# Performance work log

Measured on AMD Instinct MI355X. Metric: run time of the kernel, lower is better.

Reference implementation:

```python
import jax, jax.numpy as jnp
import numpy as np
import math

NLAT, NLON, LMAX, MMAX = 128, 256, 50, 50
K = 3  # three_nn

# ---- precompute: Clenshaw-Curtis quadrature (torch_harmonics 'equiangular') ----
def _cc_nodes_weights(n):
    Nn = n - 1
    theta = np.pi * np.arange(n) / Nn
    v = np.zeros(n)
    for k in range(1, Nn // 2 + 1):
        b = 1.0 if 2 * k == Nn else 2.0
        v += b * np.cos(2 * k * theta) / (4 * k * k - 1)
    w = (2.0 / Nn) * (1.0 - v)
    w[0] *= 0.5
    w[-1] *= 0.5
    return np.cos(theta), w

# ---- precompute: orthonormal associated Legendre P_l^m(cos theta), csphase ----
def _legpoly(lmax, mmax, cost):
    sint = np.sqrt(np.clip(1.0 - cost ** 2, 0.0, None))
    p = np.zeros((mmax, lmax, cost.shape[0]))
    pmm = np.full(cost.shape[0], np.sqrt(1.0 / (4.0 * np.pi)))
    for m in range(mmax):
        if m > 0:
            pmm = -pmm * np.sqrt((2.0 * m + 1.0) / (2.0 * m)) * sint
        p[m, m] = pmm
        if m + 1 < lmax:
            p[m, m + 1] = np.sqrt(2.0 * m + 3.0) * cost * pmm
        for l in range(m + 2, lmax):
            a = np.sqrt((4.0 * l * l - 1.0) / (l * l - m * m))
            b = np.sqrt(((2.0 * l + 1.0) * (l - 1 + m) * (l - 1 - m)) / ((2.0 * l - 3.0) * (l * l - m * m)))
            p[m, l] = a * cost * p[m, l - 1] - b * p[m, l - 2]
    return p

_cost, _w = _cc_nodes_weights(NLAT)
_PCTW = jnp.asarray((_legpoly(LMAX, MMAX, _cost) * _w[None, None, :]).astype(np.float32))  # (mmax,lmax,nlat)

_gx, _gy = np.meshgrid(np.arange(NLAT), np.arange(-NLAT, NLAT), indexing='ij')
_GRID = jnp.asarray((np.stack([_gx.ravel(), _gy.ravel()], -1) / NLAT * np.pi).astype(np.float32))  # (M,2)

_RECTW = jnp.asarray(np.exp(-(LMAX - np.arange(1, LMAX + 1)) ** 2 / (2.0 * LMAX ** 2)).astype(np.float32))  # (lmax,)


def to_spherical(coords):
    # coords: (B,N,3) -> r:(B,N), sph:(B,N,2) = [arccos(x/r), azimuth in [0,2pi)]
    sq = coords ** 2
    pn = jnp.sqrt(jnp.flip(jnp.cumsum(jnp.flip(sq, -1), -1), -1))  # pn[...,i] = ||coords[...,i:]||
    r = pn[..., 0]
    phi = jnp.arccos(coords[..., :-2] / pn[..., :-2])
    a = jnp.arccos(coords[..., -2] / pn[..., -2])
    phi_final = a + (2.0 * math.pi - 2.0 * a) * (coords[..., -1] < 0)
    return r, jnp.concatenate([phi, phi_final[..., None]], axis=-1)


def interp_to_grid(coords):
    # spherical transform + 3-NN (squared dists) + distance-weighted interpolation onto the lat/lon grid
    r, sph = to_spherical(coords)
    sph = sph.at[..., 1].add(-math.pi)
    # brute-force pairwise squared distances grid(M,2) vs sph(B,N,2): (B,M,N)
    d2 = (jnp.sum(_GRID ** 2, -1)[None, :, None] + jnp.sum(sph ** 2, -1)[:, None, :]
          - 2.0 * jnp.einsum('md,bnd->bmn', _GRID, sph))
    _, idx = jax.lax.top_k(-jax.lax.stop_gradient(d2), K)  # (B,M,K), ascending distance
    sel = jax.vmap(lambda s, i: s[i])(sph, idx)            # (B,M,K,2)
    fsel = jax.vmap(lambda f, i: f[i])(r, idx)             # (B,M,K)
    dk = jnp.sum((_GRID[None, :, None, :] - sel) ** 2, -1)  # recompute selected sq-dists (differentiable)
    w = dk / jnp.sum(dk, -1, keepdims=True)                # weights = dist / sum(dist), as in source
    return jnp.sum(fsel * w, -1).reshape(-1, NLAT, NLON)


def sht_real(x):
    # RealSHT (equiangular, ortho): rfft(norm='forward')*2pi, then Legendre*quadrature einsum; real part only
    xf = jnp.fft.rfft(x, axis=-1)[..., :MMAX] * (2.0 * math.pi / NLON)
    return jnp.einsum('bkm,mlk->blm', jnp.real(xf).astype(jnp.float32), _PCTW)  # (B,lmax,mmax)


def setup_inputs() -> dict:
    key = jax.random.key(0)
    k1, k2 = jax.random.split(key)
    pred = jax.random.normal(k1, (2, 2048, 3), dtype=jnp.float32)
    target = jax.random.normal(k2, (2, 2048, 3), dtype=jnp.float32)
    return {"pred": pred, "target": target}


def reference(pred, target):
    pc = sht_real(interp_to_grid(pred))
    tc = sht_real(interp_to_grid(target))
    return jnp.mean(jnp.sum((pc - tc) ** 2 * _RECTW[None, :, None], axis=(1, 2)))
```

## Files before the change

### kernel.cpp

```cpp
#include <hip/hip_runtime.h>
#include <math.h>

#define PI_D 3.14159265358979323846
#define PIF  3.14159265358979323846f
#define NLAT 128
#define NLON 256
#define LMAX 50
#define MMAX 50
#define NPTS 2048
#define NBT 16
#define NBA 32
#define NBIN (NBT * NBA)
#define WBIN 0.19634954084936207f
#define INVW 5.092958178940651f
#define BIG 1e30f
#define KMASK 0xFFFFF800u

__device__ float g_pctwT[(size_t)LMAX * NLAT * MMAX];
__device__ float g_fre[(size_t)4 * NLAT * MMAX];

__device__ __forceinline__ void insert3(float kf, float& k0, float& k1, float& k2) {
    float n1 = __builtin_amdgcn_fmed3f(kf, k0, k1);
    float n2 = __builtin_amdgcn_fmed3f(kf, k1, k2);
    k0 = fminf(kf, k0);
    k1 = n1;
    k2 = n2;
}

__device__ __forceinline__ float mkkey(float gt, float gl, float2 tl, int idx) {
    float dt = gt - tl.x, dl = gl - tl.y;
    float d = fmaf(dt, dt, dl * dl);
    return __uint_as_float((__float_as_uint(d) & KMASK) | (unsigned)idx);
}

__global__ __launch_bounds__(1024) void fused_main(
    const float* __restrict__ pred, const float* __restrict__ tgt,
    float* __restrict__ out) {

    __shared__ float2 s_btl[NPTS];
    __shared__ float  s_br[NPTS];
    __shared__ int    s_cnt[NBIN];
    __shared__ int    s_off[NBIN + 1];
    __shared__ float  s_row[4][NLON];
    __shared__ float  s_part[4][256];

    int bid = blockIdx.x;
    int t = threadIdx.x;

    if (bid >= 128) {
        int k = bid - 128;
        int m = t;
        if (k == 0 && m == 0) out[0] = 0.0f;
        if (m >= MMAX) return;

        double thd = PI_D * (double)k / 127.0;
        float cost = (float)cos(thd);
        float sint = (float)sin(thd);

        float c2 = (float)cos(2.0 * thd);
        float two_c2 = 2.0f * c2;
        float cp = 1.0f, cc = c2, v = 0.0f;
        for (int tt = 1; tt <= 63; ++tt) {
            v += 2.0f * cc / (float)(4 * tt * tt - 1);
            float cn = two_c2 * cc - cp;
            cp = cc;
            cc = cn;
        }
        float w = (2.0f / 127.0f) * (1.0f - v);
        if (k == 0 || k == 127) w *= 0.5f;

        float pmm = sqrtf(1.0f / (4.0f * PIF));
        for (int i = 1; i <= m; ++i)
            pmm = -pmm * sqrtf((2.0f * (float)i + 1.0f) / (2.0f * (float)i)) * sint;

        float* o = g_pctwT + (size_t)k * MMAX + m;
        for (int l = 0; l < m; ++l) o[(size_t)l * NLAT * MMAX] = 0.0f;
        o[(size_t)m * NLAT * MMAX] = pmm * w;
        float plm2 = pmm, plm1 = 0.0f;
        if (m + 1 < LMAX) {
            plm1 = sqrtf(2.0f * (float)m + 3.0f) * cost * pmm;
            o[(size_t)(m + 1) * NLAT * MMAX] = plm1 * w;
        }
        for (int l = m + 2; l < LMAX; ++l) {
            float fl = (float)l;
            float denom = fl * fl - (float)(m * m);
            float a = sqrtf((4.0f * fl * fl - 1.0f) / denom);
            float b = sqrtf(((2.0f * fl + 1.0f) * (float)(l - 1 + m) * (float)(l - 1 - m)) /
                            ((2.0f * fl - 3.0f) * denom));
            float p = a * cost * plm1 - b * plm2;
            o[(size_t)l * NLAT * MMAX] = p * w;
            plm2 = plm1;
            plm1 = p;
        }
        return;
    }

    int f = bid >> 5;
    int latb = bid & 31;
    const float* src = ((f < 2) ? pred : tgt) + (size_t)(f & 1) * NPTS * 3;

    if (t < NBIN) s_cnt[t] = 0;
    __syncthreads();

    float pth[2], paz[2], pr[2];
    int pbin[2];
#pragma unroll
    for (int i = 0; i < 2; ++i) {
        int n = t + 1024 * i;
        float x = src[3 * n], y = src[3 * n + 1], z = src[3 * n + 2];
        float s1 = z * z;
        float s2 = s1 + y * y;
        float s3 = s2 + x * x;
        float r = sqrtf(s3);
        float rho = sqrtf(s2);
        float th = acosf(x / r);
        float a = acosf(y / rho);
        float az = (z < 0.0f) ? (a + (2.0f * PIF - 2.0f * a)) : a;
        az -= PIF;
        int bt = min(max((int)(th * INVW), 0), NBT - 1);
        int ba = min(max((int)((az + PIF) * INVW), 0), NBA - 1);
        int b = bt * NBA + ba;
        pth[i] = th; paz[i] = az; pr[i] = r; pbin[i] = b;
        atomicAdd(&s_cnt[b], 1);
    }
    __syncthreads();

    if (t == 0) s_off[NBIN] = NPTS;
    if (t < 64) {
        int base = t * 8;
        int loc[8];
        int run = 0;
#pragma unroll
        for (int i = 0; i < 8; ++i) { loc[i] = run; run += s_cnt[base + i]; }
        int x = run;
#pragma unroll
        for (int d = 1; d < 64; d <<= 1) {
            int y = __shfl_up(x, d);
            if (t >= d) x += y;
        }
        int ex = x - run;
#pragma unroll
        for (int i = 0; i < 8; ++i) s_off[base + i] = ex + loc[i];
    }
    __syncthreads();
    if (t < NBIN) s_cnt[t] = s_off[t];
    __syncthreads();
#pragma unroll
    for (int i = 0; i < 2; ++i) {
        int pos = atomicAdd(&s_cnt[pbin[i]], 1);
        s_btl[pos] = make_float2(pth[i], paz[i]);
        s_br[pos] = pr[i];
    }
    __syncthreads();

    int rl = t >> 8;
    int j = t & 255;
    int lat = latb + 32 * rl;
    float gt = (float)((double)lat * PI_D / 128.0);
    float gl = (float)(((double)j - 128.0) * PI_D / 128.0);
    float glp = gl + PIF;
    int bt0 = lat >> 3;
    int ba0 = j >> 3;

    auto scan_seg = [&](int i, int i1, float& q0, float& q1, float& q2) {
        for (; i + 4 <= i1; i += 4) {
            float2 a0 = s_btl[i];
            float2 a1 = s_btl[i + 1];
            float2 a2 = s_btl[i + 2];
            float2 a3 = s_btl[i + 3];
            insert3(mkkey(gt, gl, a0, i), q0, q1, q2);
            insert3(mkkey(gt, gl, a1, i + 1), q0, q1, q2);
            insert3(mkkey(gt, gl, a2, i + 2), q0, q1, q2);
            insert3(mkkey(gt, gl, a3, i + 3), q0, q1, q2);
        }
        for (; i < i1; ++i)
            insert3(mkkey(gt, gl, s_btl[i], i), q0, q1, q2);
    };

    float k0 = BIG, k1 = BIG, k2 = BIG;
    {
        int rtl = max(bt0 - 1, 0), rth = min(bt0 + 1, NBT - 1);
        int bal = max(ba0 - 1, 0), bah = min(ba0 + 1, NBA - 1);
        for (int bt = rtl; bt <= rth; ++bt)
            scan_seg(s_off[bt * NBA + bal], s_off[bt * NBA + bah + 1], k0, k1, k2);
    }

    bool done;
    {
        float safe = BIG;
        if (bt0 - 1 > 0)       safe = fminf(safe, gt - (float)(bt0 - 1) * WBIN);
        if (bt0 + 1 < NBT - 1) safe = fminf(safe, (float)(bt0 + 2) * WBIN - gt);
        if (ba0 - 1 > 0)       safe = fminf(safe, glp - (float)(ba0 - 1) * WBIN);
        if (ba0 + 1 < NBA - 1) safe = fminf(safe, (float)(ba0 + 2) * WBIN - glp);
        done = (k2 <= safe * safe);
    }

    for (int R = 2; R <= 31; ++R) {
        if (__all(done)) break;
        if (!done) {
            int btl = bt0 - R, bth = bt0 + R;
            int lo = max(btl, 0), hi = min(bth, NBT - 1);
            int bal = max(ba0 - R, 0), bah = min(ba0 + R, NBA - 1);
            for (int bt = lo; bt <= hi; ++bt) {
                if (bt == btl || bt == bth) {
                    scan_seg(s_off[bt * NBA + bal], s_off[bt * NBA + bah + 1], k0, k1, k2);
                } else {
                    if (ba0 - R >= 0) {
                        int b = bt * NBA + ba0 - R;
                        scan_seg(s_off[b], s_off[b + 1], k0, k1, k2);
                    }
                    if (ba0 + R <= NBA - 1) {
                        int b = bt * NBA + ba0 + R;
                        scan_seg(s_off[b], s_off[b + 1], k0, k1, k2);
                    }
                }
            }
            float safe = BIG;
            if (bt0 - R > 0)       safe = fminf(safe, gt - (float)(bt0 - R) * WBIN);
            if (bt0 + R < NBT - 1) safe = fminf(safe, (float)(bt0 + R + 1) * WBIN - gt);
            if (ba0 - R > 0)       safe = fminf(safe, glp - (float)(ba0 - R) * WBIN);
            if (ba0 + R < NBA - 1) safe = fminf(safe, (float)(ba0 + R + 1) * WBIN - glp);
            if (k2 <= safe * safe) done = true;
        }
    }

    {
        int i0 = __float_as_uint(k0) & 0x7FF;
        int i1 = __float_as_uint(k1) & 0x7FF;
        int i2 = __float_as_uint(k2) & 0x7FF;
        float2 p0 = s_btl[i0];
        float2 p1 = s_btl[i1];
        float2 p2 = s_btl[i2];
        float dt0 = gt - p0.x, dl0 = gl - p0.y;
        float dt1 = gt - p1.x, dl1 = gl - p1.y;
        float dt2 = gt - p2.x, dl2 = gl - p2.y;
        float d0 = fmaf(dt0, dt0, dl0 * dl0);
        float d1 = fmaf(dt1, dt1, dl1 * dl1);
        float d2 = fmaf(dt2, dt2, dl2 * dl2);
        float s = d0 + d1 + d2;
        s_row[rl][j] = (d0 * s_br[i0] + d1 * s_br[i1] + d2 * s_br[i2]) / s;
    }
    __syncthreads();

    {
        int q = (t >> 6) & 3;
        int mm = t & 63;
        if (mm < MMAX) {
            int bs = q * 64;
            const float W0 = 2.0f * PIF / 256.0f;
            float cphi2 = 2.0f * __cosf(W0 * (float)mm);
            float acc = 0.0f;
#pragma unroll
            for (int seg = 0; seg < 4; ++seg) {
                int i0 = bs + seg * 16;
                float c0 = __cosf(W0 * (float)((i0 * mm) & 255));
                float c1 = __cosf(W0 * (float)(((i0 + 1) * mm) & 255));
                acc = fmaf(s_row[rl][i0], c0, acc);
                acc = fmaf(s_row[rl][i0 + 1], c1, acc);
#pragma unroll
                for (int i = 2; i < 16; ++i) {
                    float cn = fmaf(cphi2, c1, -c0);
                    acc = fmaf(s_row[rl][i0 + i], cn, acc);
                    c0 = c1;
                    c1 = cn;
                }
            }
            s_part[rl][q * 64 + mm] = acc;
        }
    }
    __syncthreads();
    {
        int mm = t & 255;
        if (mm < MMAX) {
            const float* pp = s_part[rl];
            float v = ((pp[mm] + pp[64 + mm]) + (pp[128 + mm] + pp[192 + mm])) *
                      (float)(2.0 * PI_D / (double)NLON);
            g_fre[(f * NLAT + lat) * MMAX + mm] = v;
        }
    }
}

__global__ __launch_bounds__(256) void contract_loss(float* __restrict__ out) {
    int b = blockIdx.x / LMAX;
    int l = blockIdx.x % LMAX;
    int mm = threadIdx.x & 63;
    int kq = threadIdx.x >> 6;
    __shared__ float sp[4][64], st_[4][64];
    float pc = 0.0f, tc = 0.0f;
    if (mm < MMAX) {
        const float* pw = g_pctwT + ((size_t)l * NLAT + kq * 32) * MMAX + mm;
        const float* fp = g_fre + ((size_t)b * NLAT + kq * 32) * MMAX + mm;
        const float* ft = g_fre + ((size_t)(2 + b) * NLAT + kq * 32) * MMAX + mm;
#pragma unroll 8
        for (int k = 0; k < 32; ++k) {
            float w = pw[k * MMAX];
            pc += fp[k * MMAX] * w;
            tc += ft[k * MMAX] * w;
        }
    }
    sp[kq][mm] = pc;
    st_[kq][mm] = tc;
    __syncthreads();
    if (threadIdx.x < 64) {
        int m2 = threadIdx.x;
        float pcs = (sp[0][m2] + sp[1][m2]) + (sp[2][m2] + sp[3][m2]);
        float tcs = (st_[0][m2] + st_[1][m2]) + (st_[2][m2] + st_[3][m2]);
        float diff = pcs - tcs;
        double dl_ = (double)(49 - l);
        float rw = (float)exp(-(dl_ * dl_) / 5000.0);
        float contrib = (m2 < MMAX) ? diff * diff * rw * 0.5f : 0.0f;
        for (int off = 32; off > 0; off >>= 1) contrib += __shfl_down(contrib, off);
        if (m2 == 0) atomicAdd(out, contrib);
    }
}

extern "C" void kernel_launch(void* const* d_in, const int* in_sizes, int n_in,
                              void* d_out, int out_size, void* d_ws, size_t ws_size,
                              hipStream_t stream) {
    const float* pred = (const float*)d_in[0];
    const float* tgt = (const float*)d_in[1];
    float* out = (float*)d_out;
    (void)d_ws; (void)ws_size;

    fused_main<<<256, 1024, 0, stream>>>(pred, tgt, out);
    contract_loss<<<2 * LMAX, 256, 0, stream>>>(out);
}
```

Baseline: 79.17 us.

## Merge contraction into main kernel using a software grid barrier

Folds the contract_loss kernel into the main kernel. All 256 blocks meet at a global atomic arrive/spin barrier, after which the first 100 blocks do the Legendre contraction and loss reduction. The departure counter resets the barrier for the next call. This removes the second kernel launch and its launch gap. In exchange it depends on all 256 blocks of 1024 threads being co-resident, which should hold on MI355X's 256 CUs but is not guaranteed, and it adds spin-wait and fence costs.

```diff
diff --git a/kernel.cpp b/kernel.cpp
--- a/kernel.cpp
+++ b/kernel.cpp
@@ -19,6 +19,9 @@
 __device__ float g_pctwT[(size_t)LMAX * NLAT * MMAX];
 __device__ float g_fre[(size_t)4 * NLAT * MMAX];
 
+__device__ int g_arrive = 0;
+__device__ int g_depart = 0;
+
 __device__ __forceinline__ void insert3(float kf, float& k0, float& k1, float& k2) {
     float n1 = __builtin_amdgcn_fmed3f(kf, k0, k1);
     float n2 = __builtin_amdgcn_fmed3f(kf, k1, k2);
@@ -33,7 +36,7 @@
     return __uint_as_float((__float_as_uint(d) & KMASK) | (unsigned)idx);
 }
 
-__global__ __launch_bounds__(1024) void fused_main(
+__global__ __launch_bounds__(1024) void fused_all(
     const float* __restrict__ pred, const float* __restrict__ tgt,
     float* __restrict__ out) {
 
@@ -43,6 +46,7 @@
     __shared__ int    s_off[NBIN + 1];
     __shared__ float  s_row[4][NLON];
     __shared__ float  s_part[4][256];
+    __shared__ float  sp[4][64], st2[4][64];
 
     int bid = blockIdx.x;
     int t = threadIdx.x;
@@ -51,266 +55,286 @@
         int k = bid - 128;
         int m = t;
         if (k == 0 && m == 0) out[0] = 0.0f;
-        if (m >= MMAX) return;
-
-        double thd = PI_D * (double)k / 127.0;
-        float cost = (float)cos(thd);
-        float sint = (float)sin(thd);
-
-        float c2 = (float)cos(2.0 * thd);
-        float two_c2 = 2.0f * c2;
-        float cp = 1.0f, cc = c2, v = 0.0f;
-        for (int tt = 1; tt <= 63; ++tt) {
-            v += 2.0f * cc / (float)(4 * tt * tt - 1);
-            float cn = two_c2 * cc - cp;
-            cp = cc;
-            cc = cn;
-        }
-        float w = (2.0f / 127.0f) * (1.0f - v);
-        if (k == 0 || k == 127) w *= 0.5f;
-
-        float pmm = sqrtf(1.0f / (4.0f * PIF));
-        for (int i = 1; i <= m; ++i)
-            pmm = -pmm * sqrtf((2.0f * (float)i + 1.0f) / (2.0f * (float)i)) * sint;
-
-        float* o = g_pctwT + (size_t)k * MMAX + m;
-        for (int l = 0; l < m; ++l) o[(size_t)l * NLAT * MMAX] = 0.0f;
-        o[(size_t)m * NLAT * MMAX] = pmm * w;
-        float plm2 = pmm, plm1 = 0.0f;
-        if (m + 1 < LMAX) {
-            plm1 = sqrtf(2.0f * (float)m + 3.0f) * cost * pmm;
-            o[(size_t)(m + 1) * NLAT * MMAX] = plm1 * w;
-        }
-        for (int l = m + 2; l < LMAX; ++l) {
-            float fl = (float)l;
-            float denom = fl * fl - (float)(m * m);
-            float a = sqrtf((4.0f * fl * fl - 1.0f) / denom);
-            float b = sqrtf(((2.0f * fl + 1.0f) * (float)(l - 1 + m) * (float)(l - 1 - m)) /
-                            ((2.0f * fl - 3.0f) * denom));
-            float p = a * cost * plm1 - b * plm2;
-            o[(size_t)l * NLAT * MMAX] = p * w;
-            plm2 = plm1;
-            plm1 = p;
-        }
-        return;
+        if (m < MMAX) {
+            double thd = PI_D * (double)k / 127.0;
+            float cost = (float)cos(thd);
+            float sint = (float)sin(thd);
+
+            float c2 = (float)cos(2.0 * thd);
+            float two_c2 = 2.0f * c2;
+            float cp = 1.0f, cc = c2, v = 0.0f;
+            for (int tt = 1; tt <= 63; ++tt) {
+                v += 2.0f * cc / (float)(4 * tt * tt - 1);
+                float cn = two_c2 * cc - cp;
+                cp = cc;
+                cc = cn;
+            }
+            float w = (2.0f / 127.0f) * (1.0f - v);
+            if (k == 0 || k == 127) w *= 0.5f;
+
+            float pmm = sqrtf(1.0f / (4.0f * PIF));
+            for (int i = 1; i <= m; ++i)
+                pmm = -pmm * sqrtf((2.0f * (float)i + 1.0f) / (2.0f * (float)i)) * sint;
+
+            float* o = g_pctwT + (size_t)k * MMAX + m;
+            for (int l = 0; l < m; ++l) o[(size_t)l * NLAT * MMAX] = 0.0f;
+            o[(size_t)m * NLAT * MMAX] = pmm * w;
+            float plm2 = pmm, plm1 = 0.0f;
+            if (m + 1 < LMAX) {
+                plm1 = sqrtf(2.0f * (float)m + 3.0f) * cost * pmm;
+                o[(size_t)(m + 1) * NLAT * MMAX] = plm1 * w;
+            }
+            for (int l = m + 2; l < LMAX; ++l) {
+                float fl = (float)l;
+                float denom = fl * fl - (float)(m * m);
+                float a = sqrtf((4.0f * fl * fl - 1.0f) / denom);
+                float b = sqrtf(((2.0f * fl + 1.0f) * (float)(l - 1 + m) * (float)(l - 1 - m)) /
+                                ((2.0f * fl - 3.0f) * denom));
+                float p = a * cost * plm1 - b * plm2;
+                o[(size_t)l * NLAT * MMAX] = p * w;
+                plm2 = plm1;
+                plm1 = p;
+            }
+        }
+    } else {
+        int f = bid >> 5;
+        int latb = bid & 31;
+        const float* src = ((f < 2) ? pred : tgt) + (size_t)(f & 1) * NPTS * 3;
+
+        if (t < NBIN) s_cnt[t] = 0;
+        __syncthreads();
+
+        float pth[2], paz[2], pr[2];
+        int pbin[2];
+#pragma unroll
+        for (int i = 0; i < 2; ++i) {
+            int n = t + 1024 * i;
+            float x = src[3 * n], y = src[3 * n + 1], z = src[3 * n + 2];
+            float s1 = z * z;
+            float s2 = s1 + y * y;
+            float s3 = s2 + x * x;
+            float r = sqrtf(s3);
+            float rho = sqrtf(s2);
+            float th = acosf(x / r);
+            float a = acosf(y / rho);
+            float az = (z < 0.0f) ? (a + (2.0f * PIF - 2.0f * a)) : a;
+            az -= PIF;
+            int bt = min(max((int)(th * INVW), 0), NBT - 1);
+            int ba = min(max((int)((az + PIF) * INVW), 0), NBA - 1);
+            int b = bt * NBA + ba;
+            pth[i] = th; paz[i] = az; pr[i] = r; pbin[i] = b;
+            atomicAdd(&s_cnt[b], 1);
+        }
+        __syncthreads();
+
+        if (t == 0) s_off[NBIN] = NPTS;
+        if (t < 64) {
+            int base = t * 8;
+            int loc[8];
+            int run = 0;
+#pragma unroll
+            for (int i = 0; i < 8; ++i) { loc[i] = run; run += s_cnt[base + i]; }
+            int x = run;
+#pragma unroll
+            for (int d = 1; d < 64; d <<= 1) {
+                int y = __shfl_up(x, d);
+                if (t >= d) x += y;
+            }
+            int ex = x - run;
+#pragma unroll
+            for (int i = 0; i < 8; ++i) s_off[base + i] = ex + loc[i];
+        }
+        __syncthreads();
+        if (t < NBIN) s_cnt[t] = s_off[t];
+        __syncthreads();
+#pragma unroll
+        for (int i = 0; i < 2; ++i) {
+            int pos = atomicAdd(&s_cnt[pbin[i]], 1);
+            s_btl[pos] = make_float2(pth[i], paz[i]);
+            s_br[pos] = pr[i];
+        }
+        __syncthreads();
+
+        int rl = t >> 8;
+        int j = t & 255;
+        int lat = latb + 32 * rl;
+        float gt = (float)((double)lat * PI_D / 128.0);
+        float gl = (float)(((double)j - 128.0) * PI_D / 128.0);
+        float glp = gl + PIF;
+        int bt0 = lat >> 3;
+        int ba0 = j >> 3;
+
+        auto scan_seg = [&](int i, int i1, float& q0, float& q1, float& q2) {
+            for (; i + 4 <= i1; i += 4) {
+                float2 a0 = s_btl[i];
+                float2 a1 = s_btl[i + 1];
+                float2 a2 = s_btl[i + 2];
+                float2 a3 = s_btl[i + 3];
+                insert3(mkkey(gt, gl, a0, i), q0, q1, q2);
+                insert3(mkkey(gt, gl, a1, i + 1), q0, q1, q2);
+                insert3(mkkey(gt, gl, a2, i + 2), q0, q1, q2);
+                insert3(mkkey(gt, gl, a3, i + 3), q0, q1, q2);
+            }
+            for (; i < i1; ++i)
+                insert3(mkkey(gt, gl, s_btl[i], i), q0, q1, q2);
+        };
+
+        float k0 = BIG, k1 = BIG, k2 = BIG;
+        {
+            int rtl = max(bt0 - 1, 0), rth = min(bt0 + 1, NBT - 1);
+            int bal = max(ba0 - 1, 0), bah = min(ba0 + 1, NBA - 1);
+            for (int bt = rtl; bt <= rth; ++bt)
+                scan_seg(s_off[bt * NBA + bal], s_off[bt * NBA + bah + 1], k0, k1, k2);
+        }
+
+        bool done;
+        {
+            float safe = BIG;
+            if (bt0 - 1 > 0)       safe = fminf(safe, gt - (float)(bt0 - 1) * WBIN);
+            if (bt0 + 1 < NBT - 1) safe = fminf(safe, (float)(bt0 + 2) * WBIN - gt);
+            if (ba0 - 1 > 0)       safe = fminf(safe, glp - (float)(ba0 - 1) * WBIN);
+            if (ba0 + 1 < NBA - 1) safe = fminf(safe, (float)(ba0 + 2) * WBIN - glp);
+            done = (k2 <= safe * safe);
+        }
+
+        for (int R = 2; R <= 31; ++R) {
+            if (__all(done)) break;
+            if (!done) {
+                int btl = bt0 - R, bth = bt0 + R;
+                int lo = max(btl, 0), hi = min(bth, NBT - 1);
+                int bal = max(ba0 - R, 0), bah = min(ba0 + R, NBA - 1);
+                for (int bt = lo; bt <= hi; ++bt) {
+                    if (bt == btl || bt == bth) {
+                        scan_seg(s_off[bt * NBA + bal], s_off[bt * NBA + bah + 1], k0, k1, k2);
+                    } else {
+                        if (ba0 - R >= 0) {
+                            int b = bt * NBA + ba0 - R;
+                            scan_seg(s_off[b], s_off[b + 1], k0, k1, k2);
+                        }
+                        if (ba0 + R <= NBA - 1) {
+                            int b = bt * NBA + ba0 + R;
+                            scan_seg(s_off[b], s_off[b + 1], k0, k1, k2);
+                        }
+                    }
+                }
+                float safe = BIG;
+                if (bt0 - R > 0)       safe = fminf(safe, gt - (float)(bt0 - R) * WBIN);
+                if (bt0 + R < NBT - 1) safe = fminf(safe, (float)(bt0 + R + 1) * WBIN - gt);
+                if (ba0 - R > 0)       safe = fminf(safe, glp - (float)(ba0 - R) * WBIN);
+                if (ba0 + R < NBA - 1) safe = fminf(safe, (float)(ba0 + R + 1) * WBIN - glp);
+                if (k2 <= safe * safe) done = true;
+            }
+        }
+
+        {
+            int i0 = __float_as_uint(k0) & 0x7FF;
+            int i1 = __float_as_uint(k1) & 0x7FF;
+            int i2 = __float_as_uint(k2) & 0x7FF;
+            float2 p0 = s_btl[i0];
+            float2 p1 = s_btl[i1];
+            float2 p2 = s_btl[i2];
+            float dt0 = gt - p0.x, dl0 = gl - p0.y;
+            float dt1 = gt - p1.x, dl1 = gl - p1.y;
+            float dt2 = gt - p2.x, dl2 = gl - p2.y;
+            float d0 = fmaf(dt0, dt0, dl0 * dl0);
+            float d1 = fmaf(dt1, dt1, dl1 * dl1);
+            float d2 = fmaf(dt2, dt2, dl2 * dl2);
+            float s = d0 + d1 + d2;
+            s_row[rl][j] = (d0 * s_br[i0] + d1 * s_br[i1] + d2 * s_br[i2]) / s;
+        }
+        __syncthreads();
+
+        {
+            int q = (t >> 6) & 3;
+            int mm = t & 63;
+            if (mm < MMAX) {
+                int bs = q * 64;
+                const float W0 = 2.0f * PIF / 256.0f;
+                float cphi2 = 2.0f * __cosf(W0 * (float)mm);
+                float acc = 0.0f;
+#pragma unroll
+                for (int seg = 0; seg < 4; ++seg) {
+                    int i0 = bs + seg * 16;
+                    float c0 = __cosf(W0 * (float)((i0 * mm) & 255));
+                    float c1 = __cosf(W0 * (float)(((i0 + 1) * mm) & 255));
+                    acc = fmaf(s_row[rl][i0], c0, acc);
+                    acc = fmaf(s_row[rl][i0 + 1], c1, acc);
+#pragma unroll
+                    for (int i = 2; i < 16; ++i) {
+                        float cn = fmaf(cphi2, c1, -c0);
+                        acc = fmaf(s_row[rl][i0 + i], cn, acc);
+                        c0 = c1;
+                        c1 = cn;
+                    }
+                }
+                s_part[rl][q * 64 + mm] = acc;
+            }
+        }
+        __syncthreads();
+        {
+            int mm = t & 255;
+            if (mm < MMAX) {
+                const float* pp = s_part[rl];
+                float v = ((pp[mm] + pp[64 + mm]) + (pp[128 + mm] + pp[192 + mm])) *
+                          (float)(2.0 * PI_D / (double)NLON);
+                g_fre[(f * NLAT + lat) * MMAX + mm] = v;
+            }
+        }
     }
 
-    int f = bid >> 5;
-    int latb = bid & 31;
-    const float* src = ((f < 2) ? pred : tgt) + (size_t)(f & 1) * NPTS * 3;
-
-    if (t < NBIN) s_cnt[t] = 0;
     __syncthreads();
-
-    float pth[2], paz[2], pr[2];
-    int pbin[2];
-#pragma unroll
-    for (int i = 0; i < 2; ++i) {
-        int n = t + 1024 * i;
-        float x = src[3 * n], y = src[3 * n + 1], z = src[3 * n + 2];
-        float s1 = z * z;
-        float s2 = s1 + y * y;
-        float s3 = s2 + x * x;
-        float r = sqrtf(s3);
-        float rho = sqrtf(s2);
-        float th = acosf(x / r);
-        float a = acosf(y / rho);
-        float az = (z < 0.0f) ? (a + (2.0f * PIF - 2.0f * a)) : a;
-        az -= PIF;
-        int bt = min(max((int)(th * INVW), 0), NBT - 1);
-        int ba = min(max((int)((az + PIF) * INVW), 0), NBA - 1);
-        int b = bt * NBA + ba;
-        pth[i] = th; paz[i] = az; pr[i] = r; pbin[i] = b;
-        atomicAdd(&s_cnt[b], 1);
+    if (t == 0) {
+        __threadfence();
+        atomicAdd(&g_arrive, 1);
+        while (__hip_atomic_load(&g_arrive, __ATOMIC_RELAXED,
+                                 __HIP_MEMORY_SCOPE_AGENT) < 256) {
+            __builtin_amdgcn_s_sleep(2);
+        }
     }
     __syncthreads();
-
-    if (t == 0) s_off[NBIN] = NPTS;
-    if (t < 64) {
-        int base = t * 8;
-        int loc[8];
-        int run = 0;
-#pragma unroll
-        for (int i = 0; i < 8; ++i) { loc[i] = run; run += s_cnt[base + i]; }
-        int x = run;
-#pragma unroll
-        for (int d = 1; d < 64; d <<= 1) {
-            int y = __shfl_up(x, d);
-            if (t >= d) x += y;
-        }
-        int ex = x - run;
-#pragma unroll
-        for (int i = 0; i < 8; ++i) s_off[base + i] = ex + loc[i];
+    __threadfence();
+
+    if (bid < 2 * LMAX) {
+        int b = bid / LMAX;
+        int l = bid % LMAX;
+        int mm = t & 63;
+        int kq = (t >> 6) & 3;
+        float pc = 0.0f, tc = 0.0f;
+        if (t < 256 && mm < MMAX) {
+            const float* pw = g_pctwT + ((size_t)l * NLAT + kq * 32) * MMAX + mm;
+            const float* fp = g_fre + ((size_t)b * NLAT + kq * 32) * MMAX + mm;
+            const float* ft = g_fre + ((size_t)(2 + b) * NLAT + kq * 32) * MMAX + mm;
+#pragma unroll 8
+            for (int k = 0; k < 32; ++k) {
+                float w = pw[k * MMAX];
+                pc += fp[k * MMAX] * w;
+                tc += ft[k * MMAX] * w;
+            }
+        }
+        if (t < 256) {
+            sp[kq][mm] = pc;
+            st2[kq][mm] = tc;
+        }
+        __syncthreads();
+        if (t < 64) {
+            int m2 = t;
+            float pcs = (sp[0][m2] + sp[1][m2]) + (sp[2][m2] + sp[3][m2]);
+            float tcs = (st2[0][m2] + st2[1][m2]) + (st2[2][m2] + st2[3][m2]);
+            float diff = pcs - tcs;
+            double dl_ = (double)(49 - l);
+            float rw = (float)exp(-(dl_ * dl_) / 5000.0);
+            float contrib = (m2 < MMAX) ? diff * diff * rw * 0.5f : 0.0f;
+            for (int off = 32; off > 0; off >>= 1) contrib += __shfl_down(contrib, off);
+            if (m2 == 0) atomicAdd(out, contrib);
+        }
     }
-    __syncthreads();
-    if (t < NBIN) s_cnt[t] = s_off[t];
-    __syncthreads();
-#pragma unroll
-    for (int i = 0; i < 2; ++i) {
-        int pos = atomicAdd(&s_cnt[pbin[i]], 1);
-        s_btl[pos] = make_float2(pth[i], paz[i]);
-        s_br[pos] = pr[i];
-    }
-    __syncthreads();
-
-    int rl = t >> 8;
-    int j = t & 255;
-    int lat = latb + 32 * rl;
-    float gt = (float)((double)lat * PI_D / 128.0);
-    float gl = (float)(((double)j - 128.0) * PI_D / 128.0);
-    float glp = gl + PIF;
-    int bt0 = lat >> 3;
-    int ba0 = j >> 3;
-
-    auto scan_seg = [&](int i, int i1, float& q0, float& q1, float& q2) {
-        for (; i + 4 <= i1; i += 4) {
-            float2 a0 = s_btl[i];
-            float2 a1 = s_btl[i + 1];
-            float2 a2 = s_btl[i + 2];
-            float2 a3 = s_btl[i + 3];
-            insert3(mkkey(gt, gl, a0, i), q0, q1, q2);
-            insert3(mkkey(gt, gl, a1, i + 1), q0, q1, q2);
-            insert3(mkkey(gt, gl, a2, i + 2), q0, q1, q2);
-            insert3(mkkey(gt, gl, a3, i + 3), q0, q1, q2);
-        }
-        for (; i < i1; ++i)
-            insert3(mkkey(gt, gl, s_btl[i], i), q0, q1, q2);
-    };
-
-    float k0 = BIG, k1 = BIG, k2 = BIG;
-    {
-        int rtl = max(bt0 - 1, 0), rth = min(bt0 + 1, NBT - 1);
-        int bal = max(ba0 - 1, 0), bah = min(ba0 + 1, NBA - 1);
-        for (int bt = rtl; bt <= rth; ++bt)
-            scan_seg(s_off[bt * NBA + bal], s_off[bt * NBA + bah + 1], k0, k1, k2);
-    }
-
-    bool done;
-    {
-        float safe = BIG;
-        if (bt0 - 1 > 0)       safe = fminf(safe, gt - (float)(bt0 - 1) * WBIN);
-        if (bt0 + 1 < NBT - 1) safe = fminf(safe, (float)(bt0 + 2) * WBIN - gt);
-        if (ba0 - 1 > 0)       safe = fminf(safe, glp - (float)(ba0 - 1) * WBIN);
-        if (ba0 + 1 < NBA - 1) safe = fminf(safe, (float)(ba0 + 2) * WBIN - glp);
-        done = (k2 <= safe * safe);
-    }
-
-    for (int R = 2; R <= 31; ++R) {
-        if (__all(done)) break;
-        if (!done) {
-            int btl = bt0 - R, bth = bt0 + R;
-            int lo = max(btl, 0), hi = min(bth, NBT - 1);
-            int bal = max(ba0 - R, 0), bah = min(ba0 + R, NBA - 1);
-            for (int bt = lo; bt <= hi; ++bt) {
-                if (bt == btl || bt == bth) {
-                    scan_seg(s_off[bt * NBA + bal], s_off[bt * NBA + bah + 1], k0, k1, k2);
-                } else {
-                    if (ba0 - R >= 0) {
-                        int b = bt * NBA + ba0 - R;
-                        scan_seg(s_off[b], s_off[b + 1], k0, k1, k2);
-                    }
-                    if (ba0 + R <= NBA - 1) {
-                        int b = bt * NBA + ba0 + R;
-                        scan_seg(s_off[b], s_off[b + 1], k0, k1, k2);
-                    }
-                }
-            }
-            float safe = BIG;
-            if (bt0 - R > 0)       safe = fminf(safe, gt - (float)(bt0 - R) * WBIN);
-            if (bt0 + R < NBT - 1) safe = fminf(safe, (float)(bt0 + R + 1) * WBIN - gt);
-            if (ba0 - R > 0)       safe = fminf(safe, glp - (float)(ba0 - R) * WBIN);
-            if (ba0 + R < NBA - 1) safe = fminf(safe, (float)(ba0 + R + 1) * WBIN - glp);
-            if (k2 <= safe * safe) done = true;
-        }
-    }
-
-    {
-        int i0 = __float_as_uint(k0) & 0x7FF;
-        int i1 = __float_as_uint(k1) & 0x7FF;
-        int i2 = __float_as_uint(k2) & 0x7FF;
-        float2 p0 = s_btl[i0];
-        float2 p1 = s_btl[i1];
-        float2 p2 = s_btl[i2];
-        float dt0 = gt - p0.x, dl0 = gl - p0.y;
-        float dt1 = gt - p1.x, dl1 = gl - p1.y;
-        float dt2 = gt - p2.x, dl2 = gl - p2.y;
-        float d0 = fmaf(dt0, dt0, dl0 * dl0);
-        float d1 = fmaf(dt1, dt1, dl1 * dl1);
-        float d2 = fmaf(dt2, dt2, dl2 * dl2);
-        float s = d0 + d1 + d2;
-        s_row[rl][j] = (d0 * s_br[i0] + d1 * s_br[i1] + d2 * s_br[i2]) / s;
-    }
-    __syncthreads();
-
-    {
-        int q = (t >> 6) & 3;
-        int mm = t & 63;
-        if (mm < MMAX) {
-            int bs = q * 64;
-            const float W0 = 2.0f * PIF / 256.0f;
-            float cphi2 = 2.0f * __cosf(W0 * (float)mm);
-            float acc = 0.0f;
-#pragma unroll
-            for (int seg = 0; seg < 4; ++seg) {
-                int i0 = bs + seg * 16;
-                float c0 = __cosf(W0 * (float)((i0 * mm) & 255));
-                float c1 = __cosf(W0 * (float)(((i0 + 1) * mm) & 255));
-                acc = fmaf(s_row[rl][i0], c0, acc);
-                acc = fmaf(s_row[rl][i0 + 1], c1, acc);
-#pragma unroll
-                for (int i = 2; i < 16; ++i) {
-                    float cn = fmaf(cphi2, c1, -c0);
-                    acc = fmaf(s_row[rl][i0 + i], cn, acc);
-                    c0 = c1;
-                    c1 = cn;
-                }
-            }
-            s_part[rl][q * 64 + mm] = acc;
-        }
-    }
-    __syncthreads();
-    {
-        int mm = t & 255;
-        if (mm < MMAX) {
-            const float* pp = s_part[rl];
-            float v = ((pp[mm] + pp[64 + mm]) + (pp[128 + mm] + pp[192 + mm])) *
-                      (float)(2.0 * PI_D / (double)NLON);
-            g_fre[(f * NLAT + lat) * MMAX + mm] = v;
-        }
-    }
-}
-
-__global__ __launch_bounds__(256) void contract_loss(float* __restrict__ out) {
-    int b = blockIdx.x / LMAX;
-    int l = blockIdx.x % LMAX;
-    int mm = threadIdx.x & 63;
-    int kq = threadIdx.x >> 6;
-    __shared__ float sp[4][64], st_[4][64];
-    float pc = 0.0f, tc = 0.0f;
-    if (mm < MMAX) {
-        const float* pw = g_pctwT + ((size_t)l * NLAT + kq * 32) * MMAX + mm;
-        const float* fp = g_fre + ((size_t)b * NLAT + kq * 32) * MMAX + mm;
-        const float* ft = g_fre + ((size_t)(2 + b) * NLAT + kq * 32) * MMAX + mm;
-#pragma unroll 8
-        for (int k = 0; k < 32; ++k) {
-            float w = pw[k * MMAX];
-            pc += fp[k * MMAX] * w;
-            tc += ft[k * MMAX] * w;
-        }
-    }
-    sp[kq][mm] = pc;
-    st_[kq][mm] = tc;
-    __syncthreads();
-    if (threadIdx.x < 64) {
-        int m2 = threadIdx.x;
-        float pcs = (sp[0][m2] + sp[1][m2]) + (sp[2][m2] + sp[3][m2]);
-        float tcs = (st_[0][m2] + st_[1][m2]) + (st_[2][m2] + st_[3][m2]);
-        float diff = pcs - tcs;
-        double dl_ = (double)(49 - l);
-        float rw = (float)exp(-(dl_ * dl_) / 5000.0);
-        float contrib = (m2 < MMAX) ? diff * diff * rw * 0.5f : 0.0f;
-        for (int off = 32; off > 0; off >>= 1) contrib += __shfl_down(contrib, off);
-        if (m2 == 0) atomicAdd(out, contrib);
+
+    if (t == 0) {
+        int d = atomicAdd(&g_depart, 1);
+        if (d == 255) {
+            __hip_atomic_store(&g_arrive, 0, __ATOMIC_RELAXED, __HIP_MEMORY_SCOPE_AGENT);
+            __hip_atomic_store(&g_depart, 0, __ATOMIC_RELAXED, __HIP_MEMORY_SCOPE_AGENT);
+        }
     }
 }
 
@@ -322,6 +346,5 @@
     float* out = (float*)d_out;
     (void)d_ws; (void)ws_size;
 
-    fused_main<<<256, 1024, 0, stream>>>(pred, tgt, out);
-    contract_loss<<<2 * LMAX, 256, 0, stream>>>(out);
+    fused_all<<<256, 1024, 0, stream>>>(pred, tgt, out);
 }
```

Measured after the change: 146.9 us. 1.86x slower.

## Split fused kernel into one-latitude-row blocks of 256 threads

Applied to the files above, without the earlier changes.

Changes the main kernel from 128 blocks of 1024 threads, each covering four latitude rows, to 512 blocks of 256 threads, each covering one row. Each thread now processes eight points in the binning phase. The goal is to fill more compute units and give each block a smaller footprint. The cost is that per-block point binning and sorting is repeated four times as often.

```diff
diff --git a/kernel.cpp b/kernel.cpp
--- a/kernel.cpp
+++ b/kernel.cpp
@@ -33,7 +33,7 @@
     return __uint_as_float((__float_as_uint(d) & KMASK) | (unsigned)idx);
 }
 
-__global__ __launch_bounds__(1024) void fused_main(
+__global__ __launch_bounds__(256) void fused_main(
     const float* __restrict__ pred, const float* __restrict__ tgt,
     float* __restrict__ out) {
 
@@ -41,14 +41,14 @@
     __shared__ float  s_br[NPTS];
     __shared__ int    s_cnt[NBIN];
     __shared__ int    s_off[NBIN + 1];
-    __shared__ float  s_row[4][NLON];
-    __shared__ float  s_part[4][256];
+    __shared__ float  s_row[NLON];
+    __shared__ float  s_part[256];
 
     int bid = blockIdx.x;
     int t = threadIdx.x;
 
-    if (bid >= 128) {
-        int k = bid - 128;
+    if (bid >= 512) {
+        int k = bid - 512;
         int m = t;
         if (k == 0 && m == 0) out[0] = 0.0f;
         if (m >= MMAX) return;
@@ -95,18 +95,18 @@
         return;
     }
 
-    int f = bid >> 5;
-    int latb = bid & 31;
+    int f = bid >> 7;
+    int lat = bid & 127;
     const float* src = ((f < 2) ? pred : tgt) + (size_t)(f & 1) * NPTS * 3;
 
-    if (t < NBIN) s_cnt[t] = 0;
-    __syncthreads();
-
-    float pth[2], paz[2], pr[2];
-    int pbin[2];
-#pragma unroll
-    for (int i = 0; i < 2; ++i) {
-        int n = t + 1024 * i;
+    for (int i = t; i < NBIN; i += 256) s_cnt[i] = 0;
+    __syncthreads();
+
+    float pth[8], paz[8], pr[8];
+    int pbin[8];
+#pragma unroll
+    for (int i = 0; i < 8; ++i) {
+        int n = t + 256 * i;
         float x = src[3 * n], y = src[3 * n + 1], z = src[3 * n + 2];
         float s1 = z * z;
         float s2 = s1 + y * y;
@@ -143,19 +143,17 @@
         for (int i = 0; i < 8; ++i) s_off[base + i] = ex + loc[i];
     }
     __syncthreads();
-    if (t < NBIN) s_cnt[t] = s_off[t];
-    __syncthreads();
-#pragma unroll
-    for (int i = 0; i < 2; ++i) {
+    for (int i = t; i < NBIN; i += 256) s_cnt[i] = s_off[i];
+    __syncthreads();
+#pragma unroll
+    for (int i = 0; i < 8; ++i) {
         int pos = atomicAdd(&s_cnt[pbin[i]], 1);
         s_btl[pos] = make_float2(pth[i], paz[i]);
         s_br[pos] = pr[i];
     }
     __syncthreads();
 
-    int rl = t >> 8;
-    int j = t & 255;
-    int lat = latb + 32 * rl;
+    int j = t;
     float gt = (float)((double)lat * PI_D / 128.0);
     float gl = (float)(((double)j - 128.0) * PI_D / 128.0);
     float glp = gl + PIF;
@@ -238,12 +236,12 @@
         float d1 = fmaf(dt1, dt1, dl1 * dl1);
         float d2 = fmaf(dt2, dt2, dl2 * dl2);
         float s = d0 + d1 + d2;
-        s_row[rl][j] = (d0 * s_br[i0] + d1 * s_br[i1] + d2 * s_br[i2]) / s;
+        s_row[j] = (d0 * s_br[i0] + d1 * s_br[i1] + d2 * s_br[i2]) / s;
     }
     __syncthreads();
 
     {
-        int q = (t >> 6) & 3;
+        int q = t >> 6;
         int mm = t & 63;
         if (mm < MMAX) {
             int bs = q * 64;
@@ -255,28 +253,25 @@
                 int i0 = bs + seg * 16;
                 float c0 = __cosf(W0 * (float)((i0 * mm) & 255));
                 float c1 = __cosf(W0 * (float)(((i0 + 1) * mm) & 255));
-                acc = fmaf(s_row[rl][i0], c0, acc);
-                acc = fmaf(s_row[rl][i0 + 1], c1, acc);
+                acc = fmaf(s_row[i0], c0, acc);
+                acc = fmaf(s_row[i0 + 1], c1, acc);
 #pragma unroll
                 for (int i = 2; i < 16; ++i) {
                     float cn = fmaf(cphi2, c1, -c0);
-                    acc = fmaf(s_row[rl][i0 + i], cn, acc);
+                    acc = fmaf(s_row[i0 + i], cn, acc);
                     c0 = c1;
                     c1 = cn;
                 }
             }
-            s_part[rl][q * 64 + mm] = acc;
-        }
-    }
-    __syncthreads();
-    {
-        int mm = t & 255;
-        if (mm < MMAX) {
-            const float* pp = s_part[rl];
-            float v = ((pp[mm] + pp[64 + mm]) + (pp[128 + mm] + pp[192 + mm])) *
-                      (float)(2.0 * PI_D / (double)NLON);
-            g_fre[(f * NLAT + lat) * MMAX + mm] = v;
-        }
+            s_part[q * 64 + mm] = acc;
+        }
+    }
+    __syncthreads();
+    if (t < MMAX) {
+        int mm = t;
+        float v = ((s_part[mm] + s_part[64 + mm]) + (s_part[128 + mm] + s_part[192 + mm])) *
+                  (float)(2.0 * PI_D / (double)NLON);
+        g_fre[(f * NLAT + lat) * MMAX + mm] = v;
     }
 }
 
@@ -322,6 +317,6 @@
     float* out = (float*)d_out;
     (void)d_ws; (void)ws_size;
 
-    fused_main<<<256, 1024, 0, stream>>>(pred, tgt, out);
+    fused_main<<<640, 256, 0, stream>>>(pred, tgt, out);
     contract_loss<<<2 * LMAX, 256, 0, stream>>>(out);
 }
```

After: 84.28 us. 6.5% more time.
